# Optimization experiments

Hardware: AMD Instinct MI355X
Metric: run time of the kernel (lower is better)

Reference implementation:

```python
import jax, jax.numpy as jnp
import numpy as np

N_NODES, IN_CH, T_IN = 2048, 64, 512
CONV_F, LSTM_H = 64, 128
NEG_BIG = -9.0e15


def conv1d(x, w, b):
    # x: [N, C_in, T], w: [C_out, C_in, 3], padding=1
    y = jax.lax.conv_general_dilated(x, w, window_strides=(1,), padding=((1, 1),),
                                     dimension_numbers=('NCH', 'OIH', 'NCH'))
    return y + b[None, :, None]


def batchnorm(x, g, b, eps=1e-5):
    # training-mode BatchNorm1d: batch stats over (N, T) per channel, biased var
    m = x.mean(axis=(0, 2), keepdims=True)
    v = x.var(axis=(0, 2), keepdims=True)
    return g[None, :, None] * (x - m) / jnp.sqrt(v + eps) + b[None, :, None]


def maxpool2(x):
    n, c, t = x.shape
    return x.reshape(n, c, t // 2, 2).max(axis=-1)


def lstm_dir(x, w_ih, w_hh, b):
    # x: [T, N, D]; gate order i, f, g, o (PyTorch convention)
    T, N, _ = x.shape
    H = w_hh.shape[1]
    pre = jnp.einsum('tnd,gd->tng', x, w_ih) + b  # [T, N, 4H]
    def step(carry, p):
        h, c = carry
        gates = p + h @ w_hh.T
        i, f, g, o = jnp.split(gates, 4, axis=-1)
        c = jax.nn.sigmoid(f) * c + jax.nn.sigmoid(i) * jnp.tanh(g)
        h = jax.nn.sigmoid(o) * jnp.tanh(c)
        return (h, c), h
    init = (jnp.zeros((N, H), x.dtype), jnp.zeros((N, H), x.dtype))
    _, hs = jax.lax.scan(step, init, pre)
    return hs  # [T, N, H]


def gat_layer(h, adj, W, a):
    # e[i,j] = leakyrelu(a . [Wh_i, Wh_j]) computed without the NxNx2F concat
    Wh = h @ W.T                      # [N, F]
    F_ = Wh.shape[1]
    s1 = Wh @ a[0, :F_]               # contribution of target node i
    s2 = Wh @ a[0, F_:]               # contribution of source node j
    e = jax.nn.leaky_relu(s1[:, None] + s2[None, :], 0.2)
    att = jax.nn.softmax(jnp.where(adj > 0, e, NEG_BIG), axis=1)
    return att @ Wh


def setup_inputs() -> dict:
    key = jax.random.key(0)
    ks = jax.random.split(key, 24)
    s = 0.05
    f32 = jnp.float32
    inp = {
        'x': jax.random.normal(ks[0], (N_NODES, IN_CH, T_IN), f32),
        'adj': jax.random.randint(ks[1], (N_NODES, N_NODES), 0, 2, jnp.int32),
        'conv1_w': s * jax.random.normal(ks[2], (CONV_F, IN_CH, 3), f32),
        'conv1_b': s * jax.random.normal(ks[3], (CONV_F,), f32),
        'bn1_g': jnp.ones((CONV_F,), f32),
        'bn1_b': jnp.zeros((CONV_F,), f32),
        'conv2_w': s * jax.random.normal(ks[4], (2 * CONV_F, CONV_F, 3), f32),
        'conv2_b': s * jax.random.normal(ks[5], (2 * CONV_F,), f32),
        'bn2_g': jnp.ones((2 * CONV_F,), f32),
        'bn2_b': jnp.zeros((2 * CONV_F,), f32),
        'wif': s * jax.random.normal(ks[6], (4 * LSTM_H, 2 * CONV_F), f32),
        'whf': s * jax.random.normal(ks[7], (4 * LSTM_H, LSTM_H), f32),
        'bf': s * jax.random.normal(ks[8], (4 * LSTM_H,), f32),
        'wir': s * jax.random.normal(ks[9], (4 * LSTM_H, 2 * CONV_F), f32),
        'whr': s * jax.random.normal(ks[10], (4 * LSTM_H, LSTM_H), f32),
        'br': s * jax.random.normal(ks[11], (4 * LSTM_H,), f32),
        'gat1_W': s * jax.random.normal(ks[12], (128, 256), f32),
        'gat1_a': s * jax.random.normal(ks[13], (1, 256), f32),
        'gat2_W': s * jax.random.normal(ks[14], (128, 128), f32),
        'gat2_a': s * jax.random.normal(ks[15], (1, 256), f32),
    }
    return inp


def reference(x, adj, conv1_w, conv1_b, bn1_g, bn1_b, conv2_w, conv2_b, bn2_g, bn2_b,
              wif, whf, bf, wir, whr, br, gat1_W, gat1_a, gat2_W, gat2_a):
    y = maxpool2(jax.nn.relu(batchnorm(conv1d(x, conv1_w, conv1_b), bn1_g, bn1_b)))
    y = maxpool2(jax.nn.relu(batchnorm(conv1d(y, conv2_w, conv2_b), bn2_g, bn2_b)))
    seq = y.transpose(2, 0, 1)                 # [T, N, 2*conv_filters]
    hf = lstm_dir(seq, wif, whf, bf)           # [T, N, H]
    hr = lstm_dir(seq[::-1], wir, whr, br)[::-1]
    feats = jnp.concatenate([hf, hr], axis=-1).mean(axis=0)  # [N, 256]
    h1 = jax.nn.elu(gat_layer(feats, adj, gat1_W, gat1_a))
    return gat_layer(h1, adj, gat2_W, gat2_a)
```

## Files before the change

### kernel.cpp

```cpp
#include <hip/hip_runtime.h>

typedef unsigned int uint;
#define DI __device__ __forceinline__

typedef __bf16 bf16;
typedef __attribute__((ext_vector_type(4))) float f32x4;
typedef __attribute__((ext_vector_type(8))) __bf16 bf16x8;
typedef __attribute__((ext_vector_type(4))) int i32x4;

constexpr size_t OFF_A    = 0;
constexpr size_t OFF_B    = 33554432;
constexpr size_t OFF_B1   = OFF_B + 16777216;
constexpr size_t OFF_WHHG = 67108864;
constexpr size_t OFF_WIHG = OFF_WHHG + 65536;
constexpr size_t OFF_BIAS = OFF_WIHG + 65536;
constexpr size_t OFF_HSUM = OFF_BIAS + 1024;
constexpr size_t OFF_FEAT = OFF_HSUM + 524288;
constexpr size_t OFF_WH1  = OFF_FEAT + 524288;
constexpr size_t OFF_S1A  = OFF_WH1 + 262144;
constexpr size_t OFF_S2A  = OFF_S1A + 2048;
constexpr size_t OFF_H1   = OFF_S2A + 2048;
constexpr size_t OFF_WH2  = OFF_H1 + 262144;
constexpr size_t OFF_S1B  = OFF_WH2 + 262144;
constexpr size_t OFF_S2B  = OFF_S1B + 2048;
constexpr size_t OFF_STAT = OFF_S2B + 2048;
constexpr size_t OFF_W1P  = OFF_STAT + 512;
constexpr size_t OFF_W2P  = OFF_W1P + 6144;
constexpr size_t OFF_WHT  = OFF_W2P + 12288;

DI float bflo(uint u){ union { uint i; float f; } v; v.i = u << 16;         return v.f; }
DI float bfhi(uint u){ union { uint i; float f; } v; v.i = u & 0xffff0000u; return v.f; }
DI float fexp2_(float x){ return __builtin_amdgcn_exp2f(x); }
DI float frcp_(float x){ return __builtin_amdgcn_rcpf(x); }
DI float sigf_(float x){ return frcp_(1.0f + fexp2_(x * -1.44269504f)); }
DI float tanhx_(float x){ return 1.0f - 2.0f*frcp_(1.0f + fexp2_(x * 2.88539009f)); }

DI f32x4 mfma16(i32x4 a, i32x4 b, f32x4 c){
  return __builtin_amdgcn_mfma_f32_16x16x32_bf16(
      __builtin_bit_cast(bf16x8, a), __builtin_bit_cast(bf16x8, b), c, 0, 0, 0);
}

DI char* swz128(char* base, int row, int byteInRow){ return base + row*128 + (byteInRow ^ ((row&7)<<4)); }
DI char* swz256(char* base, int row, int byteInRow){ return base + row*256 + (byteInRow ^ ((row&7)<<4)); }

__global__ void prep_kernel(const float* __restrict__ whf, const float* __restrict__ whr,
                            const float* __restrict__ wif, const float* __restrict__ wir,
                            const float* __restrict__ bfv, const float* __restrict__ brv,
                            const float* __restrict__ c1w, const float* __restrict__ c2w,
                            bf16* __restrict__ whh_g, bf16* __restrict__ wih_g,
                            float* __restrict__ bias_g,
                            bf16* __restrict__ w1p, bf16* __restrict__ w2p)
{
  const int dir = blockIdx.y;
  const float* whh = dir ? whr : whf;
  const float* wih = dir ? wir : wif;
  const float* bb  = dir ? brv : bfv;
  int idx = blockIdx.x*256 + threadIdx.x;
  int c = idx >> 7, d = idx & 127;
  int src = ((c & 3)*128 + (c >> 2))*128 + d;
  whh_g[(size_t)dir*65536 + idx] = (bf16)whh[src];
  wih_g[(size_t)dir*65536 + idx] = (bf16)wih[src];
  if (idx < 512) bias_g[dir*512 + idx] = bb[(idx & 3)*128 + (idx >> 2)];
  if (dir == 0) {
    if (idx < 12288) {
      int row = idx >> 6;
      int ci = (((idx & 63)*2) ^ ((row & 7) << 4)) >> 1;
      int co = row & 63, dk = row >> 6;
      w1p[idx] = (bf16)c1w[(co*64 + ci)*3 + dk];
    }
    if (idx < 24576) {
      int row = idx >> 6;
      int ci = (((idx & 63)*2) ^ ((row & 7) << 4)) >> 1;
      int co = row & 127, dk = row >> 7;
      w2p[idx] = (bf16)c2w[(co*64 + ci)*3 + dk];
    }
  }
}

__global__ __launch_bounds__(512) void conv1_kernel(
    const float* __restrict__ x, const bf16* __restrict__ w1p,
    const float* __restrict__ bias, bf16* __restrict__ y)
{
  __shared__ bf16 xa[258*64];
  __shared__ bf16 wb[3*64*64];
  const int n = blockIdx.y, t0 = blockIdx.x*256, tid = threadIdx.x;
  {
    const i32x4* wsrc = (const i32x4*)w1p;
    for (int i = tid; i < 1536; i += 512) ((i32x4*)wb)[i] = wsrc[i];
  }
  for (int i = tid; i < 2048; i += 512) {
    int q = i & 63, cp = i >> 6;
    int ci = cp*2;
    const float* xb = &x[((size_t)n*64 + ci)*512 + t0 + q*4];
    float4 v0 = *(const float4*)xb;
    float4 v1 = *(const float4*)(xb + 512);
    int row = q*4 + 1;
    union { bf16 h[2]; uint u; } p0, p1, p2, p3;
    p0.h[0]=(bf16)v0.x; p0.h[1]=(bf16)v1.x;
    p1.h[0]=(bf16)v0.y; p1.h[1]=(bf16)v1.y;
    p2.h[0]=(bf16)v0.z; p2.h[1]=(bf16)v1.z;
    p3.h[0]=(bf16)v0.w; p3.h[1]=(bf16)v1.w;
    *(uint*)swz128((char*)xa, row+0, ci*2) = p0.u;
    *(uint*)swz128((char*)xa, row+1, ci*2) = p1.u;
    *(uint*)swz128((char*)xa, row+2, ci*2) = p2.u;
    *(uint*)swz128((char*)xa, row+3, ci*2) = p3.u;
  }
  if (tid < 128) {
    int ci = tid >> 1, e = tid & 1;
    int row = e ? 257 : 0;
    int t = t0 + (e ? 256 : -1);
    float v = (t >= 0 && t < 512) ? x[((size_t)n*64 + ci)*512 + t] : 0.0f;
    *(bf16*)swz128((char*)xa, row, ci*2) = (bf16)v;
  }
  __syncthreads();
  const int lane = tid & 63, wv = tid >> 6;
  const int m0 = (wv & 3)*64, c0 = (wv >> 2)*32;
  const int l15 = lane & 15, lh = lane >> 4;
  f32x4 acc[4][2];
  #pragma unroll
  for (int mf = 0; mf < 4; ++mf)
    #pragma unroll
    for (int cf = 0; cf < 2; ++cf) {
      float bb = bias[c0 + cf*16 + l15];
      acc[mf][cf] = (f32x4){bb, bb, bb, bb};
    }
  #pragma unroll
  for (int dk = 0; dk < 3; ++dk)
    #pragma unroll
    for (int ks = 0; ks < 2; ++ks) {
      const int kb = ks*64 + lh*16;
      i32x4 bfr[2], afr[4];
      #pragma unroll
      for (int cf = 0; cf < 2; ++cf) {
        int row = dk*64 + c0 + cf*16 + l15;
        bfr[cf] = *(const i32x4*)swz128((char*)wb, row, kb);
      }
      #pragma unroll
      for (int mf = 0; mf < 4; ++mf) {
        int row = m0 + mf*16 + l15 + dk;
        afr[mf] = *(const i32x4*)swz128((char*)xa, row, kb);
      }
      #pragma unroll
      for (int mf = 0; mf < 4; ++mf)
        #pragma unroll
        for (int cf = 0; cf < 2; ++cf)
          acc[mf][cf] = mfma16(afr[mf], bfr[cf], acc[mf][cf]);
    }
  #pragma unroll
  for (int mf = 0; mf < 4; ++mf)
    #pragma unroll
    for (int cf = 0; cf < 2; ++cf) {
      int co = c0 + cf*16 + l15;
      int tt = t0 + m0 + mf*16 + lh*4;
      union { bf16 h[4]; uint2 u; } pk;
      #pragma unroll
      for (int r = 0; r < 4; ++r) pk.h[r] = (bf16)acc[mf][cf][r];
      *(uint2*)&y[((size_t)n*64 + co)*512 + tt] = pk.u;
    }
}

__global__ __launch_bounds__(512) void conv2_kernel(
    const bf16* __restrict__ xin, const bf16* __restrict__ w2p,
    const float* __restrict__ bias, bf16* __restrict__ y)
{
  __shared__ bf16 xa[258*64];
  __shared__ bf16 wb[3*128*64];
  const int n = blockIdx.x, tid = threadIdx.x;
  {
    const i32x4* wsrc = (const i32x4*)w2p;
    for (int i = tid; i < 3072; i += 512) ((i32x4*)wb)[i] = wsrc[i];
  }
  {
    const i32x4* src = (const i32x4*)(xin + (size_t)n*256*64);
    for (int i = tid; i < 2048; i += 512) {
      int row = (i >> 3) + 1, blk = i & 7;
      *(i32x4*)swz128((char*)xa, row, blk*16) = src[i];
    }
  }
  if (tid < 128) {
    int ci = tid >> 1, e = tid & 1;
    int row = e ? 257 : 0;
    *(bf16*)swz128((char*)xa, row, ci*2) = (bf16)0.0f;
  }
  __syncthreads();
  const int lane = tid & 63, wv = tid >> 6;
  const int m0 = (wv & 3)*64, c0 = (wv >> 2)*64;
  const int l15 = lane & 15, lh = lane >> 4;
  f32x4 acc[4][4];
  #pragma unroll
  for (int mf = 0; mf < 4; ++mf)
    #pragma unroll
    for (int cf = 0; cf < 4; ++cf) {
      float bb = bias[c0 + cf*16 + l15];
      acc[mf][cf] = (f32x4){bb, bb, bb, bb};
    }
  #pragma unroll
  for (int dk = 0; dk < 3; ++dk)
    #pragma unroll
    for (int ks = 0; ks < 2; ++ks) {
      const int kb = ks*64 + lh*16;
      i32x4 bfr[4], afr[4];
      #pragma unroll
      for (int cf = 0; cf < 4; ++cf) {
        int row = dk*128 + c0 + cf*16 + l15;
        bfr[cf] = *(const i32x4*)swz128((char*)wb, row, kb);
      }
      #pragma unroll
      for (int mf = 0; mf < 4; ++mf) {
        int row = m0 + mf*16 + l15 + dk;
        afr[mf] = *(const i32x4*)swz128((char*)xa, row, kb);
      }
      #pragma unroll
      for (int mf = 0; mf < 4; ++mf)
        #pragma unroll
        for (int cf = 0; cf < 4; ++cf)
          acc[mf][cf] = mfma16(afr[mf], bfr[cf], acc[mf][cf]);
    }
  #pragma unroll
  for (int mf = 0; mf < 4; ++mf)
    #pragma unroll
    for (int cf = 0; cf < 4; ++cf) {
      int co = c0 + cf*16 + l15;
      int tt = m0 + mf*16 + lh*4;
      union { bf16 h[4]; uint2 u; } pk;
      #pragma unroll
      for (int r = 0; r < 4; ++r) pk.h[r] = (bf16)acc[mf][cf][r];
      *(uint2*)&y[((size_t)n*128 + co)*256 + tt] = pk.u;
    }
}

__global__ __launch_bounds__(256) void bn_stats_kernel(
    const bf16* __restrict__ y, float* __restrict__ stat, int C, int T)
{
  const int c = blockIdx.x, n0 = blockIdx.y*64, tid = threadIdx.x;
  float s = 0.f, q = 0.f;
  const int qpr = T >> 3;
  for (int i = tid; i < 64*qpr; i += 256) {
    int n = n0 + i/qpr, qd = i & (qpr - 1);
    uint4 u = *(const uint4*)&y[((size_t)n*C + c)*T + qd*8];
    float v0 = bflo(u.x), v1 = bfhi(u.x), v2 = bflo(u.y), v3 = bfhi(u.y);
    float v4 = bflo(u.z), v5 = bfhi(u.z), v6 = bflo(u.w), v7 = bfhi(u.w);
    s += (v0+v1)+(v2+v3)+((v4+v5)+(v6+v7));
    q += (v0*v0+v1*v1)+(v2*v2+v3*v3)+((v4*v4+v5*v5)+(v6*v6+v7*v7));
  }
  __shared__ float rs[256], rq[256];
  rs[tid] = s; rq[tid] = q; __syncthreads();
  for (int off = 128; off > 0; off >>= 1) {
    if (tid < off) { rs[tid] += rs[tid+off]; rq[tid] += rq[tid+off]; }
    __syncthreads();
  }
  if (tid == 0) { atomicAdd(&stat[c], rs[0]); atomicAdd(&stat[128+c], rq[0]); }
}

__global__ void bn_finalize_kernel(float* __restrict__ stat, const float* __restrict__ g,
                                   const float* __restrict__ b, int C, float invCnt)
{
  int c = threadIdx.x;
  if (c < C) {
    float m  = stat[c]*invCnt;
    float v  = stat[128+c]*invCnt - m*m;
    float sc = g[c]*rsqrtf(v + 1e-5f);
    stat[256+c] = sc;
    stat[384+c] = b[c] - m*sc;
  }
}

template<int C, int TH>
__global__ __launch_bounds__(256) void poolT_kernel(
    const bf16* __restrict__ yin, const float* __restrict__ stat, bf16* __restrict__ outp)
{
  __shared__ bf16 buf[C][TH + 2];
  const int n = blockIdx.x, tid = threadIdx.x;
  const uint* src = (const uint*)(yin + (size_t)n*C*TH*2);
  for (int i = tid; i < C*TH; i += 256) {
    int th = i & (TH - 1), c = i / TH;
    uint u = src[i];
    float sc = stat[256 + c], sh = stat[384 + c];
    float a = fmaxf(sc*bflo(u) + sh, 0.f);
    float b = fmaxf(sc*bfhi(u) + sh, 0.f);
    buf[c][th] = (bf16)fmaxf(a, b);
  }
  __syncthreads();
  bf16* dst = outp + (size_t)n*TH*C;
  for (int i = tid; i < TH*C/2; i += 256) {
    int cp = i & (C/2 - 1), th = i / (C/2);
    union { bf16 h[2]; uint u; } pk;
    pk.h[0] = buf[2*cp][th]; pk.h[1] = buf[2*cp + 1][th];
    *(uint*)&dst[th*C + 2*cp] = pk.u;
  }
}

__global__ __launch_bounds__(512, 2) void lstm_fused_kernel(
    const bf16* __restrict__ p2t, const bf16* __restrict__ wih_g,
    const bf16* __restrict__ whh_g, const float* __restrict__ bias_g,
    float* __restrict__ hsum)
{
  __shared__ bf16 hb[2][2048];
  const int z = blockIdx.x;
  const int dir = z & 1, n0 = (z >> 1)*16;
  const int tid = threadIdx.x, lane = tid & 63, wv = tid >> 6;
  const int l15 = lane & 15, lh = lane >> 4;
  i32x4 wihr[4][4], whhr[4][4];
  {
    const bf16* wi = wih_g + (size_t)dir*65536;
    const bf16* wh = whh_g + (size_t)dir*65536;
    #pragma unroll
    for (int cf = 0; cf < 4; ++cf) {
      int c = wv*64 + cf*16 + l15;
      #pragma unroll
      for (int ks = 0; ks < 4; ++ks) {
        wihr[cf][ks] = *(const i32x4*)(wi + (size_t)c*128 + ks*32 + lh*8);
        whhr[cf][ks] = *(const i32x4*)(wh + (size_t)c*128 + ks*32 + lh*8);
      }
    }
  }
  f32x4 bias4[4];
  #pragma unroll
  for (int cf = 0; cf < 4; ++cf) {
    int hh = wv*16 + cf*4 + lh;
    bias4[cf] = *(const f32x4*)&bias_g[dir*512 + hh*4];
  }
  for (int i = tid; i < 256; i += 512) ((i32x4*)hb[0])[i] = (i32x4){0,0,0,0};
  const bf16* xrow = p2t + (size_t)(n0 + l15)*128*128;
  float creg[4] = {0.f,0.f,0.f,0.f}, hac[4] = {0.f,0.f,0.f,0.f};
  f32x4 acc[4];
  i32x4 xn[4];
  {
    int ts0 = dir ? 127 : 0;
    #pragma unroll
    for (int ks = 0; ks < 4; ++ks)
      xn[ks] = *(const i32x4*)(xrow + (size_t)ts0*128 + ks*32 + lh*8);
    #pragma unroll
    for (int cf = 0; cf < 4; ++cf) {
      acc[cf] = mfma16(wihr[cf][0], xn[0], bias4[cf]);
      #pragma unroll
      for (int ks = 1; ks < 4; ++ks)
        acc[cf] = mfma16(wihr[cf][ks], xn[ks], acc[cf]);
    }
  }
  int cur = 0;
  __syncthreads();
  for (int t = 0; t < 128; ++t) {
    {
      int tn = (t + 1 < 128) ? t + 1 : 127;
      int tsn = dir ? 127 - tn : tn;
      #pragma unroll
      for (int ks = 0; ks < 4; ++ks)
        xn[ks] = *(const i32x4*)(xrow + (size_t)tsn*128 + ks*32 + lh*8);
    }
    {
      i32x4 a0 = *(const i32x4*)swz256((char*)hb[cur], l15, 0*64 + lh*16);
      i32x4 a1 = *(const i32x4*)swz256((char*)hb[cur], l15, 1*64 + lh*16);
      #pragma unroll
      for (int cf = 0; cf < 4; ++cf) {
        acc[cf] = mfma16(whhr[cf][0], a0, acc[cf]);
        acc[cf] = mfma16(whhr[cf][1], a1, acc[cf]);
      }
      a0 = *(const i32x4*)swz256((char*)hb[cur], l15, 2*64 + lh*16);
      a1 = *(const i32x4*)swz256((char*)hb[cur], l15, 3*64 + lh*16);
      #pragma unroll
      for (int cf = 0; cf < 4; ++cf) {
        acc[cf] = mfma16(whhr[cf][2], a0, acc[cf]);
        acc[cf] = mfma16(whhr[cf][3], a1, acc[cf]);
      }
    }
    #pragma unroll
    for (int cf = 0; cf < 4; ++cf) {
      float ig = sigf_(acc[cf][0]);
      float fg = sigf_(acc[cf][1]);
      float gg = tanhx_(acc[cf][2]);
      float og = sigf_(acc[cf][3]);
      float cv = fg*creg[cf] + ig*gg;
      creg[cf] = cv;
      float hv = og*tanhx_(cv);
      hac[cf] += hv;
      int hh = wv*16 + cf*4 + lh;
      *(bf16*)swz256((char*)hb[cur^1], l15, hh*2) = (bf16)hv;
    }
    #pragma unroll
    for (int cf = 0; cf < 4; ++cf) {
      acc[cf] = mfma16(wihr[cf][0], xn[0], bias4[cf]);
      #pragma unroll
      for (int ks = 1; ks < 4; ++ks)
        acc[cf] = mfma16(wihr[cf][ks], xn[ks], acc[cf]);
    }
    __syncthreads();
    cur ^= 1;
  }
  float* hm = hsum + ((size_t)dir*2048 + n0)*128;
  #pragma unroll
  for (int cf = 0; cf < 4; ++cf) {
    int hh = wv*16 + cf*4 + lh;
    hm[(size_t)l15*128 + hh] = hac[cf];
  }
}

__global__ __launch_bounds__(256) void feats_kernel(const float* __restrict__ hsum, float* __restrict__ feats)
{
  int idx = blockIdx.x*256 + threadIdx.x;
  int k = idx & 255, n = idx >> 8;
  float v = (k < 128) ? hsum[(size_t)n*128 + k]
                      : hsum[(size_t)2048*128 + (size_t)n*128 + (k - 128)];
  feats[idx] = v * 0.0078125f;
}

template<int K>
__global__ __launch_bounds__(256) void node_gemm_kernel(
    const float* __restrict__ inp, const float* __restrict__ W,
    float* __restrict__ outp, bf16* __restrict__ outT)
{
  __shared__ float ft[32][K];
  const int i0 = blockIdx.x*32, tid = threadIdx.x;
  for (int i = tid; i < 32*K; i += 256) ft[i/K][i%K] = inp[(size_t)i0*K + i];
  __syncthreads();
  const int f = tid & 127, ih = (tid >> 7)*16;
  float acc[16];
  #pragma unroll
  for (int ii = 0; ii < 16; ++ii) acc[ii] = 0.f;
  const float* wp = W + (size_t)f*K;
  for (int k = 0; k < K; k += 4) {
    const float4 wv = *reinterpret_cast<const float4*>(&wp[k]);
    #pragma unroll
    for (int ii = 0; ii < 16; ++ii) {
      const float* fp = &ft[ih+ii][k];
      acc[ii] += fp[0]*wv.x + fp[1]*wv.y + fp[2]*wv.z + fp[3]*wv.w;
    }
  }
  union { bf16 h[16]; uint4 u[2]; } pk;
  #pragma unroll
  for (int ii = 0; ii < 16; ++ii) {
    outp[(size_t)(i0+ih+ii)*128 + f] = acc[ii];
    pk.h[ii] = (bf16)acc[ii];
  }
  uint4* dT = (uint4*)&outT[(size_t)f*2048 + i0 + ih];
  dT[0] = pk.u[0]; dT[1] = pk.u[1];
}

__global__ __launch_bounds__(256) void gat_s_kernel(const float* __restrict__ Wh,
    const float* __restrict__ a, float* __restrict__ s1, float* __restrict__ s2)
{
  const int node = blockIdx.x*4 + (threadIdx.x >> 6);
  const int l = threadIdx.x & 63;
  const float w0 = Wh[(size_t)node*128 + l], w1 = Wh[(size_t)node*128 + 64 + l];
  float v1 = w0*a[l]     + w1*a[64+l];
  float v2 = w0*a[128+l] + w1*a[192+l];
  #pragma unroll
  for (int off = 32; off > 0; off >>= 1) { v1 += __shfl_down(v1, off); v2 += __shfl_down(v2, off); }
  if (l == 0) { s1[node] = v1; s2[node] = v2; }
}

__global__ __launch_bounds__(512) void gat_attn16_kernel(
    const bf16* __restrict__ WhT,
    const float* __restrict__ s1, const float* __restrict__ s2v,
    const int* __restrict__ adj, float* __restrict__ outp, int applyElu)
{
  __shared__ bf16 P[16*2048];
  __shared__ float sums[16];
  const int i0 = blockIdx.x*16, tid = threadIdx.x;
  const int lane = tid & 63, w = tid >> 6;
  for (int rr = 0; rr < 2; ++rr) {
    const int r = w*2 + rr, i = i0 + r;
    const float s1i = s1[i];
    const int4* arow = (const int4*)(adj + (size_t)i*2048);
    float ev[8][4];
    float m = -3.0e38f;
    #pragma unroll
    for (int k = 0; k < 8; ++k) {
      int4 ad = arow[k*64 + lane];
      float4 sv = *(const float4*)&s2v[k*256 + lane*4];
      float e0 = s1i + sv.x; e0 = (e0 > 0.f) ? e0 : 0.2f*e0; e0 = (ad.x > 0) ? e0 : -3.0e38f;
      float e1 = s1i + sv.y; e1 = (e1 > 0.f) ? e1 : 0.2f*e1; e1 = (ad.y > 0) ? e1 : -3.0e38f;
      float e2 = s1i + sv.z; e2 = (e2 > 0.f) ? e2 : 0.2f*e2; e2 = (ad.z > 0) ? e2 : -3.0e38f;
      float e3 = s1i + sv.w; e3 = (e3 > 0.f) ? e3 : 0.2f*e3; e3 = (ad.w > 0) ? e3 : -3.0e38f;
      ev[k][0]=e0; ev[k][1]=e1; ev[k][2]=e2; ev[k][3]=e3;
      m = fmaxf(m, fmaxf(fmaxf(e0,e1), fmaxf(e2,e3)));
    }
    #pragma unroll
    for (int off = 32; off > 0; off >>= 1) m = fmaxf(m, __shfl_xor(m, off));
    float s = 0.f;
    char* prow = (char*)P + r*4096;
    #pragma unroll
    for (int k = 0; k < 8; ++k) {
      float p0 = __expf(ev[k][0] - m);
      float p1 = __expf(ev[k][1] - m);
      float p2 = __expf(ev[k][2] - m);
      float p3 = __expf(ev[k][3] - m);
      s += (p0+p1)+(p2+p3);
      union { bf16 h[4]; uint2 u; } pk;
      pk.h[0]=(bf16)p0; pk.h[1]=(bf16)p1; pk.h[2]=(bf16)p2; pk.h[3]=(bf16)p3;
      *(uint2*)(prow + ((k*512 + lane*8) ^ ((r&7)<<4))) = pk.u;
    }
    #pragma unroll
    for (int off = 32; off > 0; off >>= 1) s += __shfl_xor(s, off);
    if (lane == 0) sums[r] = s;
  }
  __syncthreads();
  const int l15 = lane & 15, lh = lane >> 4;
  const bf16* bT = WhT + (size_t)(w*16 + l15)*2048;
  f32x4 ac[4];
  #pragma unroll
  for (int q = 0; q < 4; ++q) ac[q] = (f32x4){0.f,0.f,0.f,0.f};
  for (int kt = 0; kt < 64; kt += 4) {
    #pragma unroll
    for (int q = 0; q < 4; ++q) {
      i32x4 af = *(const i32x4*)((char*)P + l15*4096 + (((kt+q)*64 + lh*16) ^ ((l15&7)<<4)));
      i32x4 bf = *(const i32x4*)(bT + (kt+q)*32 + lh*8);
      ac[q] = mfma16(af, bf, ac[q]);
    }
  }
  f32x4 accv = (ac[0] + ac[1]) + (ac[2] + ac[3]);
  #pragma unroll
  for (int rg = 0; rg < 4; ++rg) {
    int i = i0 + lh*4 + rg;
    float v = accv[rg] / sums[lh*4 + rg];
    if (applyElu) v = (v > 0.f) ? v : (__expf(v) - 1.0f);
    outp[(size_t)i*128 + w*16 + l15] = v;
  }
}

extern "C" void kernel_launch(void* const* d_in, const int* in_sizes, int n_in,
                              void* d_out, int out_size, void* d_ws, size_t ws_size,
                              hipStream_t stream)
{
  (void)in_sizes; (void)n_in; (void)out_size; (void)ws_size;
  const float* x    = (const float*)d_in[0];
  const int*   adj  = (const int*)d_in[1];
  const float* c1w  = (const float*)d_in[2];
  const float* c1b  = (const float*)d_in[3];
  const float* bn1g = (const float*)d_in[4];
  const float* bn1b = (const float*)d_in[5];
  const float* c2w  = (const float*)d_in[6];
  const float* c2b  = (const float*)d_in[7];
  const float* bn2g = (const float*)d_in[8];
  const float* bn2b = (const float*)d_in[9];
  const float* wif  = (const float*)d_in[10];
  const float* whf  = (const float*)d_in[11];
  const float* bfv  = (const float*)d_in[12];
  const float* wir  = (const float*)d_in[13];
  const float* whr  = (const float*)d_in[14];
  const float* brv  = (const float*)d_in[15];
  const float* g1W  = (const float*)d_in[16];
  const float* g1a  = (const float*)d_in[17];
  const float* g2W  = (const float*)d_in[18];
  const float* g2a  = (const float*)d_in[19];
  float* outp = (float*)d_out;
  float* ws   = (float*)d_ws;

  bf16* y12    = (bf16*)(ws + OFF_A);
  bf16* pool1t = (bf16*)(ws + OFF_B);
  bf16* pool2t = (bf16*)(ws + OFF_B1);
  bf16* whh_g  = (bf16*)(ws + OFF_WHHG);
  bf16* wih_g  = (bf16*)(ws + OFF_WIHG);
  float* bias_g= ws + OFF_BIAS;
  float* hsm   = ws + OFF_HSUM;
  float* feats = ws + OFF_FEAT;
  float* Wh1   = ws + OFF_WH1;
  float* s1a   = ws + OFF_S1A;
  float* s2a   = ws + OFF_S2A;
  float* h1    = ws + OFF_H1;
  float* Wh2   = ws + OFF_WH2;
  float* s1b   = ws + OFF_S1B;
  float* s2b   = ws + OFF_S2B;
  float* stat  = ws + OFF_STAT;
  bf16* w1p    = (bf16*)(ws + OFF_W1P);
  bf16* w2p    = (bf16*)(ws + OFF_W2P);
  bf16* whT    = (bf16*)(ws + OFF_WHT);

  hipMemsetAsync(stat, 0, 512*sizeof(float), stream);

  prep_kernel<<<dim3(256,2),256,0,stream>>>(whf, whr, wif, wir, bfv, brv, c1w, c2w,
                                            whh_g, wih_g, bias_g, w1p, w2p);

  conv1_kernel<<<dim3(2,2048),512,0,stream>>>(x, w1p, c1b, y12);
  bn_stats_kernel<<<dim3(64,32),256,0,stream>>>(y12, stat, 64, 512);
  bn_finalize_kernel<<<1,128,0,stream>>>(stat, bn1g, bn1b, 64, 1.0f/(2048.0f*512.0f));
  poolT_kernel<64,256><<<2048,256,0,stream>>>(y12, stat, pool1t);

  hipMemsetAsync(stat, 0, 256*sizeof(float), stream);
  conv2_kernel<<<2048,512,0,stream>>>(pool1t, w2p, c2b, y12);
  bn_stats_kernel<<<dim3(128,32),256,0,stream>>>(y12, stat, 128, 256);
  bn_finalize_kernel<<<1,128,0,stream>>>(stat, bn2g, bn2b, 128, 1.0f/(2048.0f*256.0f));
  poolT_kernel<128,128><<<2048,256,0,stream>>>(y12, stat, pool2t);

  lstm_fused_kernel<<<256,512,0,stream>>>(pool2t, wih_g, whh_g, bias_g, hsm);
  feats_kernel<<<2048,256,0,stream>>>(hsm, feats);

  node_gemm_kernel<256><<<64,256,0,stream>>>(feats, g1W, Wh1, whT);
  gat_s_kernel<<<512,256,0,stream>>>(Wh1, g1a, s1a, s2a);
  gat_attn16_kernel<<<128,512,0,stream>>>(whT, s1a, s2a, adj, h1, 1);
  node_gemm_kernel<128><<<64,256,0,stream>>>(h1, g2W, Wh2, whT);
  gat_s_kernel<<<512,256,0,stream>>>(Wh2, g2a, s1b, s2b);
  gat_attn16_kernel<<<128,512,0,stream>>>(whT, s1b, s2b, adj, outp, 0);
}
```

Before: 607.3 us.

## Fuse BN statistics into persistent double-buffered conv kernels; halve GAT attention rows per block

Both conv kernels become persistent: 256 blocks each loop over 8 nodes, loading the weights into shared memory once and double-buffering input staging. Each kernel accumulates per-channel sum and sum-of-squares in registers and writes them to 32 partitioned stat rows. This removes the separate bn_stats pass that re-read the conv output, and the finalize kernel now sums the partitions. GAT attention blocks now handle 8 rows instead of 16, doubling the grid to 256 blocks for more parallelism, but half of each MFMA tile is wasted on duplicated rows.

```diff
diff --git a/kernel.cpp b/kernel.cpp
--- a/kernel.cpp
+++ b/kernel.cpp
@@ -27,6 +27,7 @@
 constexpr size_t OFF_W1P  = OFF_STAT + 512;
 constexpr size_t OFF_W2P  = OFF_W1P + 6144;
 constexpr size_t OFF_WHT  = OFF_W2P + 12288;
+constexpr size_t OFF_STATP= OFF_WHT + 131072;
 
 DI float bflo(uint u){ union { uint i; float f; } v; v.i = u << 16;         return v.f; }
 DI float bfhi(uint u){ union { uint i; float f; } v; v.i = u & 0xffff0000u; return v.f; }
@@ -79,186 +80,218 @@
 
 __global__ __launch_bounds__(512) void conv1_kernel(
     const float* __restrict__ x, const bf16* __restrict__ w1p,
-    const float* __restrict__ bias, bf16* __restrict__ y)
-{
-  __shared__ bf16 xa[258*64];
-  __shared__ bf16 wb[3*64*64];
-  const int n = blockIdx.y, t0 = blockIdx.x*256, tid = threadIdx.x;
+    const float* __restrict__ bias, bf16* __restrict__ y, float* __restrict__ statp)
+{
+  __shared__ bf16 xa[2][16512];
+  __shared__ bf16 wb[12288];
+  __shared__ float redS[64], redQ[64];
+  const int tid = threadIdx.x, nb = blockIdx.x*8;
   {
     const i32x4* wsrc = (const i32x4*)w1p;
     for (int i = tid; i < 1536; i += 512) ((i32x4*)wb)[i] = wsrc[i];
-  }
-  for (int i = tid; i < 2048; i += 512) {
-    int q = i & 63, cp = i >> 6;
-    int ci = cp*2;
-    const float* xb = &x[((size_t)n*64 + ci)*512 + t0 + q*4];
-    float4 v0 = *(const float4*)xb;
-    float4 v1 = *(const float4*)(xb + 512);
-    int row = q*4 + 1;
-    union { bf16 h[2]; uint u; } p0, p1, p2, p3;
-    p0.h[0]=(bf16)v0.x; p0.h[1]=(bf16)v1.x;
-    p1.h[0]=(bf16)v0.y; p1.h[1]=(bf16)v1.y;
-    p2.h[0]=(bf16)v0.z; p2.h[1]=(bf16)v1.z;
-    p3.h[0]=(bf16)v0.w; p3.h[1]=(bf16)v1.w;
-    *(uint*)swz128((char*)xa, row+0, ci*2) = p0.u;
-    *(uint*)swz128((char*)xa, row+1, ci*2) = p1.u;
-    *(uint*)swz128((char*)xa, row+2, ci*2) = p2.u;
-    *(uint*)swz128((char*)xa, row+3, ci*2) = p3.u;
-  }
-  if (tid < 128) {
-    int ci = tid >> 1, e = tid & 1;
-    int row = e ? 257 : 0;
-    int t = t0 + (e ? 256 : -1);
-    float v = (t >= 0 && t < 512) ? x[((size_t)n*64 + ci)*512 + t] : 0.0f;
-    *(bf16*)swz128((char*)xa, row, ci*2) = (bf16)v;
-  }
+    if (tid < 64) { redS[tid] = 0.f; redQ[tid] = 0.f; }
+  }
+  auto stage = [&](int buf, int n, int t0) {
+    char* base = (char*)xa[buf];
+    for (int i = tid; i < 2048; i += 512) {
+      int q = i & 63, cp = i >> 6;
+      int ci = cp*2;
+      const float* xb = &x[((size_t)n*64 + ci)*512 + t0 + q*4];
+      float4 v0 = *(const float4*)xb;
+      float4 v1 = *(const float4*)(xb + 512);
+      int row = q*4 + 1;
+      union { bf16 h[2]; uint u; } p0, p1, p2, p3;
+      p0.h[0]=(bf16)v0.x; p0.h[1]=(bf16)v1.x;
+      p1.h[0]=(bf16)v0.y; p1.h[1]=(bf16)v1.y;
+      p2.h[0]=(bf16)v0.z; p2.h[1]=(bf16)v1.z;
+      p3.h[0]=(bf16)v0.w; p3.h[1]=(bf16)v1.w;
+      *(uint*)swz128(base, row+0, ci*2) = p0.u;
+      *(uint*)swz128(base, row+1, ci*2) = p1.u;
+      *(uint*)swz128(base, row+2, ci*2) = p2.u;
+      *(uint*)swz128(base, row+3, ci*2) = p3.u;
+    }
+    if (tid < 128) {
+      int ci = tid >> 1, e = tid & 1;
+      int row = e ? 257 : 0;
+      int t = t0 + (e ? 256 : -1);
+      float v = (t >= 0 && t < 512) ? x[((size_t)n*64 + ci)*512 + t] : 0.0f;
+      *(bf16*)swz128(base, row, ci*2) = (bf16)v;
+    }
+  };
+  stage(0, nb, 0);
   __syncthreads();
   const int lane = tid & 63, wv = tid >> 6;
   const int m0 = (wv & 3)*64, c0 = (wv >> 2)*32;
   const int l15 = lane & 15, lh = lane >> 4;
-  f32x4 acc[4][2];
-  #pragma unroll
-  for (int mf = 0; mf < 4; ++mf)
-    #pragma unroll
-    for (int cf = 0; cf < 2; ++cf) {
-      float bb = bias[c0 + cf*16 + l15];
-      acc[mf][cf] = (f32x4){bb, bb, bb, bb};
-    }
-  #pragma unroll
-  for (int dk = 0; dk < 3; ++dk)
-    #pragma unroll
-    for (int ks = 0; ks < 2; ++ks) {
-      const int kb = ks*64 + lh*16;
-      i32x4 bfr[2], afr[4];
+  const float bb0 = bias[c0 + l15], bb1 = bias[c0 + 16 + l15];
+  float bnS[2] = {0.f,0.f}, bnQ[2] = {0.f,0.f};
+  for (int it = 0; it < 16; ++it) {
+    const int n = nb + (it >> 1), t0 = (it & 1)*256, buf = it & 1;
+    if (it + 1 < 16) stage(buf ^ 1, nb + ((it + 1) >> 1), ((it + 1) & 1)*256);
+    char* xb = (char*)xa[buf];
+    f32x4 acc[4][2];
+    #pragma unroll
+    for (int mf = 0; mf < 4; ++mf) {
+      acc[mf][0] = (f32x4){bb0, bb0, bb0, bb0};
+      acc[mf][1] = (f32x4){bb1, bb1, bb1, bb1};
+    }
+    #pragma unroll
+    for (int dk = 0; dk < 3; ++dk)
+      #pragma unroll
+      for (int ks = 0; ks < 2; ++ks) {
+        const int kb = ks*64 + lh*16;
+        i32x4 bfr[2], afr[4];
+        #pragma unroll
+        for (int cf = 0; cf < 2; ++cf) {
+          int row = dk*64 + c0 + cf*16 + l15;
+          bfr[cf] = *(const i32x4*)swz128((char*)wb, row, kb);
+        }
+        #pragma unroll
+        for (int mf = 0; mf < 4; ++mf) {
+          int row = m0 + mf*16 + l15 + dk;
+          afr[mf] = *(const i32x4*)swz128(xb, row, kb);
+        }
+        #pragma unroll
+        for (int mf = 0; mf < 4; ++mf)
+          #pragma unroll
+          for (int cf = 0; cf < 2; ++cf)
+            acc[mf][cf] = mfma16(afr[mf], bfr[cf], acc[mf][cf]);
+      }
+    #pragma unroll
+    for (int mf = 0; mf < 4; ++mf)
       #pragma unroll
       for (int cf = 0; cf < 2; ++cf) {
-        int row = dk*64 + c0 + cf*16 + l15;
-        bfr[cf] = *(const i32x4*)swz128((char*)wb, row, kb);
+        int co = c0 + cf*16 + l15;
+        int tt = t0 + m0 + mf*16 + lh*4;
+        union { bf16 h[4]; uint2 u; } pk;
+        #pragma unroll
+        for (int r = 0; r < 4; ++r) {
+          float v = acc[mf][cf][r];
+          pk.h[r] = (bf16)v;
+          bnS[cf] += v; bnQ[cf] += v*v;
+        }
+        *(uint2*)&y[((size_t)n*64 + co)*512 + tt] = pk.u;
       }
-      #pragma unroll
-      for (int mf = 0; mf < 4; ++mf) {
-        int row = m0 + mf*16 + l15 + dk;
-        afr[mf] = *(const i32x4*)swz128((char*)xa, row, kb);
-      }
-      #pragma unroll
-      for (int mf = 0; mf < 4; ++mf)
-        #pragma unroll
-        for (int cf = 0; cf < 2; ++cf)
-          acc[mf][cf] = mfma16(afr[mf], bfr[cf], acc[mf][cf]);
-    }
-  #pragma unroll
-  for (int mf = 0; mf < 4; ++mf)
-    #pragma unroll
-    for (int cf = 0; cf < 2; ++cf) {
-      int co = c0 + cf*16 + l15;
-      int tt = t0 + m0 + mf*16 + lh*4;
-      union { bf16 h[4]; uint2 u; } pk;
-      #pragma unroll
-      for (int r = 0; r < 4; ++r) pk.h[r] = (bf16)acc[mf][cf][r];
-      *(uint2*)&y[((size_t)n*64 + co)*512 + tt] = pk.u;
-    }
+    __syncthreads();
+  }
+  atomicAdd(&redS[c0 + l15], bnS[0]);      atomicAdd(&redQ[c0 + l15], bnQ[0]);
+  atomicAdd(&redS[c0 + 16 + l15], bnS[1]); atomicAdd(&redQ[c0 + 16 + l15], bnQ[1]);
+  __syncthreads();
+  if (tid < 64) {
+    float* row = statp + (size_t)(blockIdx.x & 31)*256;
+    atomicAdd(&row[tid], redS[tid]);
+    atomicAdd(&row[128 + tid], redQ[tid]);
+  }
 }
 
 __global__ __launch_bounds__(512) void conv2_kernel(
     const bf16* __restrict__ xin, const bf16* __restrict__ w2p,
-    const float* __restrict__ bias, bf16* __restrict__ y)
-{
-  __shared__ bf16 xa[258*64];
-  __shared__ bf16 wb[3*128*64];
-  const int n = blockIdx.x, tid = threadIdx.x;
+    const float* __restrict__ bias, bf16* __restrict__ y, float* __restrict__ statp)
+{
+  __shared__ bf16 xa[2][16512];
+  __shared__ bf16 wb[24576];
+  __shared__ float redS[128], redQ[128];
+  const int tid = threadIdx.x, nb = blockIdx.x*8;
   {
     const i32x4* wsrc = (const i32x4*)w2p;
     for (int i = tid; i < 3072; i += 512) ((i32x4*)wb)[i] = wsrc[i];
-  }
-  {
-    const i32x4* src = (const i32x4*)(xin + (size_t)n*256*64);
+    if (tid < 128) { redS[tid] = 0.f; redQ[tid] = 0.f; }
+    if (tid < 256) {
+      int ci = (tid & 127) >> 1, e = tid & 1, buf = tid >> 7;
+      int row = e ? 257 : 0;
+      *(bf16*)swz128((char*)xa[buf], row, ci*2) = (bf16)0.0f;
+    }
+  }
+  auto stage = [&](int buf, int n) {
+    char* base = (char*)xa[buf];
+    const i32x4* src = (const i32x4*)(xin + (size_t)n*16384);
     for (int i = tid; i < 2048; i += 512) {
       int row = (i >> 3) + 1, blk = i & 7;
-      *(i32x4*)swz128((char*)xa, row, blk*16) = src[i];
-    }
-  }
-  if (tid < 128) {
-    int ci = tid >> 1, e = tid & 1;
-    int row = e ? 257 : 0;
-    *(bf16*)swz128((char*)xa, row, ci*2) = (bf16)0.0f;
-  }
+      *(i32x4*)swz128(base, row, blk*16) = src[i];
+    }
+  };
+  stage(0, nb);
   __syncthreads();
   const int lane = tid & 63, wv = tid >> 6;
   const int m0 = (wv & 3)*64, c0 = (wv >> 2)*64;
   const int l15 = lane & 15, lh = lane >> 4;
-  f32x4 acc[4][4];
-  #pragma unroll
-  for (int mf = 0; mf < 4; ++mf)
-    #pragma unroll
-    for (int cf = 0; cf < 4; ++cf) {
-      float bb = bias[c0 + cf*16 + l15];
-      acc[mf][cf] = (f32x4){bb, bb, bb, bb};
-    }
-  #pragma unroll
-  for (int dk = 0; dk < 3; ++dk)
-    #pragma unroll
-    for (int ks = 0; ks < 2; ++ks) {
-      const int kb = ks*64 + lh*16;
-      i32x4 bfr[4], afr[4];
+  float bbv[4];
+  #pragma unroll
+  for (int cf = 0; cf < 4; ++cf) bbv[cf] = bias[c0 + cf*16 + l15];
+  float bnS[4] = {0.f,0.f,0.f,0.f}, bnQ[4] = {0.f,0.f,0.f,0.f};
+  for (int it = 0; it < 8; ++it) {
+    const int n = nb + it, buf = it & 1;
+    if (it + 1 < 8) stage(buf ^ 1, nb + it + 1);
+    char* xb = (char*)xa[buf];
+    f32x4 acc[4][4];
+    #pragma unroll
+    for (int mf = 0; mf < 4; ++mf)
+      #pragma unroll
+      for (int cf = 0; cf < 4; ++cf)
+        acc[mf][cf] = (f32x4){bbv[cf], bbv[cf], bbv[cf], bbv[cf]};
+    #pragma unroll
+    for (int dk = 0; dk < 3; ++dk)
+      #pragma unroll
+      for (int ks = 0; ks < 2; ++ks) {
+        const int kb = ks*64 + lh*16;
+        i32x4 bfr[4], afr[4];
+        #pragma unroll
+        for (int cf = 0; cf < 4; ++cf) {
+          int row = dk*128 + c0 + cf*16 + l15;
+          bfr[cf] = *(const i32x4*)swz128((char*)wb, row, kb);
+        }
+        #pragma unroll
+        for (int mf = 0; mf < 4; ++mf) {
+          int row = m0 + mf*16 + l15 + dk;
+          afr[mf] = *(const i32x4*)swz128(xb, row, kb);
+        }
+        #pragma unroll
+        for (int mf = 0; mf < 4; ++mf)
+          #pragma unroll
+          for (int cf = 0; cf < 4; ++cf)
+            acc[mf][cf] = mfma16(afr[mf], bfr[cf], acc[mf][cf]);
+      }
+    #pragma unroll
+    for (int mf = 0; mf < 4; ++mf)
       #pragma unroll
       for (int cf = 0; cf < 4; ++cf) {
-        int row = dk*128 + c0 + cf*16 + l15;
-        bfr[cf] = *(const i32x4*)swz128((char*)wb, row, kb);
+        int co = c0 + cf*16 + l15;
+        int tt = m0 + mf*16 + lh*4;
+        union { bf16 h[4]; uint2 u; } pk;
+        #pragma unroll
+        for (int r = 0; r < 4; ++r) {
+          float v = acc[mf][cf][r];
+          pk.h[r] = (bf16)v;
+          bnS[cf] += v; bnQ[cf] += v*v;
+        }
+        *(uint2*)&y[((size_t)n*128 + co)*256 + tt] = pk.u;
       }
-      #pragma unroll
-      for (int mf = 0; mf < 4; ++mf) {
-        int row = m0 + mf*16 + l15 + dk;
-        afr[mf] = *(const i32x4*)swz128((char*)xa, row, kb);
-      }
-      #pragma unroll
-      for (int mf = 0; mf < 4; ++mf)
-        #pragma unroll
-        for (int cf = 0; cf < 4; ++cf)
-          acc[mf][cf] = mfma16(afr[mf], bfr[cf], acc[mf][cf]);
-    }
-  #pragma unroll
-  for (int mf = 0; mf < 4; ++mf)
-    #pragma unroll
-    for (int cf = 0; cf < 4; ++cf) {
-      int co = c0 + cf*16 + l15;
-      int tt = m0 + mf*16 + lh*4;
-      union { bf16 h[4]; uint2 u; } pk;
-      #pragma unroll
-      for (int r = 0; r < 4; ++r) pk.h[r] = (bf16)acc[mf][cf][r];
-      *(uint2*)&y[((size_t)n*128 + co)*256 + tt] = pk.u;
-    }
-}
-
-__global__ __launch_bounds__(256) void bn_stats_kernel(
-    const bf16* __restrict__ y, float* __restrict__ stat, int C, int T)
-{
-  const int c = blockIdx.x, n0 = blockIdx.y*64, tid = threadIdx.x;
-  float s = 0.f, q = 0.f;
-  const int qpr = T >> 3;
-  for (int i = tid; i < 64*qpr; i += 256) {
-    int n = n0 + i/qpr, qd = i & (qpr - 1);
-    uint4 u = *(const uint4*)&y[((size_t)n*C + c)*T + qd*8];
-    float v0 = bflo(u.x), v1 = bfhi(u.x), v2 = bflo(u.y), v3 = bfhi(u.y);
-    float v4 = bflo(u.z), v5 = bfhi(u.z), v6 = bflo(u.w), v7 = bfhi(u.w);
-    s += (v0+v1)+(v2+v3)+((v4+v5)+(v6+v7));
-    q += (v0*v0+v1*v1)+(v2*v2+v3*v3)+((v4*v4+v5*v5)+(v6*v6+v7*v7));
-  }
-  __shared__ float rs[256], rq[256];
-  rs[tid] = s; rq[tid] = q; __syncthreads();
-  for (int off = 128; off > 0; off >>= 1) {
-    if (tid < off) { rs[tid] += rs[tid+off]; rq[tid] += rq[tid+off]; }
     __syncthreads();
   }
-  if (tid == 0) { atomicAdd(&stat[c], rs[0]); atomicAdd(&stat[128+c], rq[0]); }
-}
-
-__global__ void bn_finalize_kernel(float* __restrict__ stat, const float* __restrict__ g,
-                                   const float* __restrict__ b, int C, float invCnt)
+  #pragma unroll
+  for (int cf = 0; cf < 4; ++cf) {
+    int co = c0 + cf*16 + l15;
+    atomicAdd(&redS[co], bnS[cf]);
+    atomicAdd(&redQ[co], bnQ[cf]);
+  }
+  __syncthreads();
+  if (tid < 128) {
+    float* row = statp + (size_t)(blockIdx.x & 31)*256;
+    atomicAdd(&row[tid], redS[tid]);
+    atomicAdd(&row[128 + tid], redQ[tid]);
+  }
+}
+
+__global__ void bn_finalize_kernel(const float* __restrict__ statp, float* __restrict__ stat,
+                                   const float* __restrict__ g, const float* __restrict__ b,
+                                   int C, float invCnt)
 {
   int c = threadIdx.x;
   if (c < C) {
-    float m  = stat[c]*invCnt;
-    float v  = stat[128+c]*invCnt - m*m;
+    float s = 0.f, q = 0.f;
+    for (int r = 0; r < 32; ++r) { s += statp[r*256 + c]; q += statp[r*256 + 128 + c]; }
+    float m  = s*invCnt;
+    float v  = q*invCnt - m*m;
     float sc = g[c]*rsqrtf(v + 1e-5f);
     stat[256+c] = sc;
     stat[384+c] = b[c] - m*sc;
@@ -449,17 +482,17 @@
   if (l == 0) { s1[node] = v1; s2[node] = v2; }
 }
 
-__global__ __launch_bounds__(512) void gat_attn16_kernel(
+__global__ __launch_bounds__(512) void gat_attn8_kernel(
     const bf16* __restrict__ WhT,
     const float* __restrict__ s1, const float* __restrict__ s2v,
     const int* __restrict__ adj, float* __restrict__ outp, int applyElu)
 {
-  __shared__ bf16 P[16*2048];
-  __shared__ float sums[16];
-  const int i0 = blockIdx.x*16, tid = threadIdx.x;
+  __shared__ bf16 P[8*2048];
+  __shared__ float sums[8];
+  const int i0 = blockIdx.x*8, tid = threadIdx.x;
   const int lane = tid & 63, w = tid >> 6;
-  for (int rr = 0; rr < 2; ++rr) {
-    const int r = w*2 + rr, i = i0 + r;
+  {
+    const int r = w, i = i0 + r;
     const float s1i = s1[i];
     const int4* arow = (const int4*)(adj + (size_t)i*2048);
     float ev[8][4];
@@ -496,6 +529,7 @@
   }
   __syncthreads();
   const int l15 = lane & 15, lh = lane >> 4;
+  const int pr = l15 & 7;
   const bf16* bT = WhT + (size_t)(w*16 + l15)*2048;
   f32x4 ac[4];
   #pragma unroll
@@ -503,18 +537,20 @@
   for (int kt = 0; kt < 64; kt += 4) {
     #pragma unroll
     for (int q = 0; q < 4; ++q) {
-      i32x4 af = *(const i32x4*)((char*)P + l15*4096 + (((kt+q)*64 + lh*16) ^ ((l15&7)<<4)));
+      i32x4 af = *(const i32x4*)((char*)P + pr*4096 + (((kt+q)*64 + lh*16) ^ ((pr&7)<<4)));
       i32x4 bf = *(const i32x4*)(bT + (kt+q)*32 + lh*8);
       ac[q] = mfma16(af, bf, ac[q]);
     }
   }
   f32x4 accv = (ac[0] + ac[1]) + (ac[2] + ac[3]);
-  #pragma unroll
-  for (int rg = 0; rg < 4; ++rg) {
-    int i = i0 + lh*4 + rg;
-    float v = accv[rg] / sums[lh*4 + rg];
-    if (applyElu) v = (v > 0.f) ? v : (__expf(v) - 1.0f);
-    outp[(size_t)i*128 + w*16 + l15] = v;
+  if (lh < 2) {
+    #pragma unroll
+    for (int rg = 0; rg < 4; ++rg) {
+      int row = lh*4 + rg;
+      float v = accv[rg] / sums[row];
+      if (applyElu) v = (v > 0.f) ? v : (__expf(v) - 1.0f);
+      outp[(size_t)(i0 + row)*128 + w*16 + l15] = v;
+    }
   }
 }
 
@@ -565,21 +601,19 @@
   bf16* w1p    = (bf16*)(ws + OFF_W1P);
   bf16* w2p    = (bf16*)(ws + OFF_W2P);
   bf16* whT    = (bf16*)(ws + OFF_WHT);
-
-  hipMemsetAsync(stat, 0, 512*sizeof(float), stream);
+  float* statp = ws + OFF_STATP;
 
   prep_kernel<<<dim3(256,2),256,0,stream>>>(whf, whr, wif, wir, bfv, brv, c1w, c2w,
                                             whh_g, wih_g, bias_g, w1p, w2p);
 
-  conv1_kernel<<<dim3(2,2048),512,0,stream>>>(x, w1p, c1b, y12);
-  bn_stats_kernel<<<dim3(64,32),256,0,stream>>>(y12, stat, 64, 512);
-  bn_finalize_kernel<<<1,128,0,stream>>>(stat, bn1g, bn1b, 64, 1.0f/(2048.0f*512.0f));
+  hipMemsetAsync(statp, 0, 8192*sizeof(float), stream);
+  conv1_kernel<<<256,512,0,stream>>>(x, w1p, c1b, y12, statp);
+  bn_finalize_kernel<<<1,128,0,stream>>>(statp, stat, bn1g, bn1b, 64, 1.0f/(2048.0f*512.0f));
   poolT_kernel<64,256><<<2048,256,0,stream>>>(y12, stat, pool1t);
 
-  hipMemsetAsync(stat, 0, 256*sizeof(float), stream);
-  conv2_kernel<<<2048,512,0,stream>>>(pool1t, w2p, c2b, y12);
-  bn_stats_kernel<<<dim3(128,32),256,0,stream>>>(y12, stat, 128, 256);
-  bn_finalize_kernel<<<1,128,0,stream>>>(stat, bn2g, bn2b, 128, 1.0f/(2048.0f*256.0f));
+  hipMemsetAsync(statp, 0, 8192*sizeof(float), stream);
+  conv2_kernel<<<256,512,0,stream>>>(pool1t, w2p, c2b, y12, statp);
+  bn_finalize_kernel<<<1,128,0,stream>>>(statp, stat, bn2g, bn2b, 128, 1.0f/(2048.0f*256.0f));
   poolT_kernel<128,128><<<2048,256,0,stream>>>(y12, stat, pool2t);
 
   lstm_fused_kernel<<<256,512,0,stream>>>(pool2t, wih_g, whh_g, bias_g, hsm);
@@ -587,8 +621,8 @@
 
   node_gemm_kernel<256><<<64,256,0,stream>>>(feats, g1W, Wh1, whT);
   gat_s_kernel<<<512,256,0,stream>>>(Wh1, g1a, s1a, s2a);
-  gat_attn16_kernel<<<128,512,0,stream>>>(whT, s1a, s2a, adj, h1, 1);
+  gat_attn8_kernel<<<256,512,0,stream>>>(whT, s1a, s2a, adj, h1, 1);
   node_gemm_kernel<128><<<64,256,0,stream>>>(h1, g2W, Wh2, whT);
   gat_s_kernel<<<512,256,0,stream>>>(Wh2, g2a, s1b, s2b);
-  gat_attn16_kernel<<<128,512,0,stream>>>(whT, s1b, s2b, adj, outp, 0);
-}
+  gat_attn8_kernel<<<256,512,0,stream>>>(whT, s1b, s2b, adj, outp, 0);
+}
```

Result: faster. 558.6 us (-8.0%).
